# Kernel optimization log

Measured on AMD Instinct MI355X. Metric: run time of the kernel, lower is better.

## Reference

```python
import jax, jax.numpy as jnp
import numpy as np

N, F_IN, H, C, E, G, OUT = 50000, 128, 4, 64, 800000, 128, 8

def _glorot(key, shape):
    lim = float(np.sqrt(6.0 / (shape[0] + shape[-1] if len(shape) == 2 else shape[-1] + 1)))
    return jax.random.uniform(key, shape, jnp.float32, -lim, lim)

def setup_inputs() -> dict:
    key = jax.random.key(0)
    ks = jax.random.split(key, 12)
    x = jax.random.normal(ks[0], (N, F_IN), jnp.float32)
    edge_index = jax.random.randint(ks[1], (2, E), 0, N, jnp.int64)
    batch = jnp.sort(jax.random.randint(ks[2], (N,), 0, G, jnp.int64))
    return {
        "x": x, "edge_index": edge_index, "batch": batch,
        "W1": _glorot(ks[3], (F_IN, H * C)),
        "a1s": _glorot(ks[4], (H, C)), "a1d": _glorot(ks[5], (H, C)),
        "b1": jnp.zeros((H * C,), jnp.float32),
        "W2": _glorot(ks[6], (H * C, H * C)),
        "a2s": _glorot(ks[7], (H, C)), "a2d": _glorot(ks[8], (H, C)),
        "b2": jnp.zeros((C,), jnp.float32),
        "fc_w": _glorot(ks[9], (C, OUT)),
        "fc_b": jnp.zeros((OUT,), jnp.float32),
    }

def _gat_conv(x, src, dst, W, a_src, a_dst, bias, concat):
    # x: [N, in]; src/dst: [E'] (self-loops already appended, PyG default)
    n = x.shape[0]
    h = (x @ W).reshape(n, H, C)                       # [N, H, C]
    alpha_src = (h * a_src).sum(-1)                    # [N, H]
    alpha_dst = (h * a_dst).sum(-1)                    # [N, H]
    e = alpha_src[src] + alpha_dst[dst]                # [E', H]
    e = jax.nn.leaky_relu(e, 0.2)
    # neighbor softmax grouped by destination node
    m = jax.ops.segment_max(e, dst, num_segments=n)    # [N, H]
    ex = jnp.exp(e - m[dst])
    denom = jax.ops.segment_sum(ex, dst, num_segments=n)
    alpha = ex / (denom[dst] + 1e-16)                  # [E', H]
    msg = h[src] * alpha[:, :, None]                   # [E', H, C]
    out = jax.ops.segment_sum(msg, dst, num_segments=n)  # [N, H, C]
    out = out.reshape(n, H * C) if concat else out.mean(axis=1)
    return out + bias

def reference(x, edge_index, batch, W1, a1s, a1d, b1, W2, a2s, a2d, b2, fc_w, fc_b):
    n = x.shape[0]
    loop = jnp.arange(n, dtype=edge_index.dtype)
    src = jnp.concatenate([edge_index[0], loop])
    dst = jnp.concatenate([edge_index[1], loop])
    h = _gat_conv(x, src, dst, W1, a1s, a1d, b1, concat=True)
    h = jax.nn.elu(h)                                  # activation, dropout p=0
    h = _gat_conv(h, src, dst, W2, a2s, a2d, b2, concat=False)
    # global mean pool over graphs
    sums = jax.ops.segment_sum(h, batch, num_segments=G)
    cnts = jax.ops.segment_sum(jnp.ones((n,), h.dtype), batch, num_segments=G)
    pooled = sums / jnp.maximum(cnts, 1.0)[:, None]    # [G, C]
    return pooled @ fc_w + fc_b                        # [G, OUT]
```

## Files before the change

kernel.cpp:

```cpp
#include <hip/hip_runtime.h>
#include <hip/hip_bf16.h>
#include <cstddef>
#include <cstdint>

#define NN 50000
#define MPAD 50048
#define F_IN 128
#define NH 4
#define NC 64
#define NE 800000
#define NG 128
#define NOUT 8
#define HC 256
#define EP (NE + NN)

typedef unsigned short ushort_t;
typedef _Float16 f16;
typedef __attribute__((ext_vector_type(2))) _Float16 f16x2;
typedef __attribute__((ext_vector_type(8))) _Float16 f16x8;
typedef __attribute__((ext_vector_type(4))) float f32x4;

__device__ __forceinline__ float lrelu02(float x) { return x > 0.0f ? x : 0.2f * x; }
__device__ __forceinline__ float elu1(float x)    { return x > 0.0f ? x : expm1f(x); }

__device__ __forceinline__ ushort_t f2h_bits(float f) {
    f16 h = (f16)f;
    union { f16 h; ushort_t u; } cv; cv.h = h;
    return cv.u;
}
__device__ __forceinline__ uint32_t pack2h(float a, float b) {
    union { f16 h[2]; uint32_t u; } cv;
    cv.h[0] = (f16)a; cv.h[1] = (f16)b;
    return cv.u;
}
__device__ __forceinline__ f16x2 as_h2(uint32_t q) {
    union { uint32_t u; f16x2 h; } cv; cv.u = q;
    return cv.h;
}
__device__ __forceinline__ void h2_unpack(uint32_t q, float& lo, float& hi) {
    union { uint32_t u; f16 h[2]; } cv; cv.u = q;
    lo = (float)cv.h[0];
    hi = (float)cv.h[1];
}

__device__ __forceinline__ float fdot2f(f16x2 a, f16x2 b, float c) {
#if __has_builtin(__builtin_amdgcn_fdot2)
    return __builtin_amdgcn_fdot2(a, b, c, false);
#else
    float d;
    asm("v_dot2_f32_f16 %0, %1, %2, %3" : "=v"(d) : "v"(a), "v"(b), "v"(c));
    return d;
#endif
}
__device__ __forceinline__ uint32_t permb(uint32_t a, uint32_t b, uint32_t s) {
    return __builtin_amdgcn_perm(a, b, s);
}
#define SEL_E 0x01000504u
#define SEL_O 0x03020706u

__device__ __forceinline__ void gld16(const void* g, void* l) {
    __builtin_amdgcn_global_load_lds(
        (const __attribute__((address_space(1))) unsigned int*)g,
        (__attribute__((address_space(3))) unsigned int*)l, 16, 0, 0);
}

#define XN4 (NN * F_IN / 4)
#define NW (F_IN * HC + HC * HC)
__global__ void prep_kernel(const int* __restrict__ edst,
                            const float* __restrict__ x,
                            const float* __restrict__ W1,
                            const float* __restrict__ W2,
                            int* __restrict__ deg,
                            f16* __restrict__ xh,
                            f16* __restrict__ w1t, f16* __restrict__ w2t) {
    int idx = blockIdx.x * blockDim.x + threadIdx.x;
    if (idx < EP) {
        int d = (idx < NE) ? edst[idx] : (idx - NE);
        atomicAdd(&deg[d], 1);
        return;
    }
    idx -= EP;
    if (idx < XN4) {
        float4 v = ((const float4*)x)[idx];
        f16 o[4] = {(f16)v.x, (f16)v.y, (f16)v.z, (f16)v.w};
        *(uint2*)(xh + idx * 4) = *(const uint2*)o;
        return;
    }
    idx -= XN4;
    const int n1 = F_IN * HC;
    if (idx < n1) {
        int k = idx / HC, n = idx % HC;
        w1t[n * F_IN + k] = (f16)W1[idx];
    } else if (idx < NW) {
        int i2 = idx - n1;
        int k = i2 / HC, n = i2 % HC;
        w2t[n * HC + k] = (f16)W2[i2];
    }
}

__global__ __launch_bounds__(256) void scan_p1(const int* __restrict__ deg,
                                               int* __restrict__ partials) {
    __shared__ int lds[256];
    int b = blockIdx.x, t = threadIdx.x;
    int i0 = b * 1024 + t * 4;
    int s = 0;
#pragma unroll
    for (int j = 0; j < 4; j++) { int i = i0 + j; if (i < NN) s += deg[i]; }
    lds[t] = s;
    __syncthreads();
    for (int o = 128; o; o >>= 1) { if (t < o) lds[t] += lds[t + o]; __syncthreads(); }
    if (t == 0) partials[b] = lds[0];
}

__global__ __launch_bounds__(256) void scan_p3(const int* __restrict__ deg,
                                               const int* __restrict__ partials,
                                               int* __restrict__ offs) {
    __shared__ int lds[256];
    __shared__ int base_s;
    int b = blockIdx.x, t = threadIdx.x;
    if (t == 0) {
        int s = 0;
        for (int i = 0; i < b; i++) s += partials[i];
        base_s = s;
        if (b == 0) offs[0] = 0;
    }
    int i0 = b * 1024 + t * 4;
    int v[4]; int s = 0;
#pragma unroll
    for (int j = 0; j < 4; j++) { int i = i0 + j; v[j] = (i < NN) ? deg[i] : 0; s += v[j]; }
    lds[t] = s;
    __syncthreads();
    for (int o = 1; o < 256; o <<= 1) {
        int x = (t >= o) ? lds[t - o] : 0;
        __syncthreads();
        lds[t] += x;
        __syncthreads();
    }
    int run = base_s + (lds[t] - s);
#pragma unroll
    for (int j = 0; j < 4; j++) { run += v[j]; int i = i0 + j; if (i < NN) offs[i + 1] = run; }
}

__global__ void edge_fill(const int* __restrict__ esrc, const int* __restrict__ edst,
                          const int* __restrict__ offs, int* __restrict__ fill,
                          int* __restrict__ csr) {
    int e = blockIdx.x * blockDim.x + threadIdx.x;
    if (e >= EP) return;
    int s, d;
    if (e < NE) { s = esrc[e]; d = edst[e]; } else { s = d = e - NE; }
    int pos = offs[d] + atomicAdd(&fill[d], 1);
    csr[pos] = s;
}

__global__ __launch_bounds__(256, 3) void gemm_gat(
        const f16* __restrict__ A, const f16* __restrict__ BT,
        const float* __restrict__ a_s, const float* __restrict__ a_d,
        ushort_t* __restrict__ hf2, float* __restrict__ asrc,
        float* __restrict__ adst, int M, int K) {
    __shared__ alignas(16) char smem[33792];
    f16* lA = (f16*)smem;
    f16* lB = (f16*)smem + 4096;

    int t = threadIdx.x;
    int wave = t >> 6, lane = t & 63;
    int wm = wave >> 1, wn = wave & 1;
    int quad = lane >> 4, l15 = lane & 15;
    int tileM = blockIdx.x * 128;
    int by = blockIdx.y;

    f32x4 acc[4][4];
#pragma unroll
    for (int f = 0; f < 4; f++)
#pragma unroll
        for (int g = 0; g < 4; g++) acc[f][g] = (f32x4){0.f, 0.f, 0.f, 0.f};

    for (int k0 = 0; k0 < K; k0 += 32) {
        __syncthreads();
#pragma unroll
        for (int i = 0; i < 2; i++) {
            int c = wave * 2 + i;
            int row = c * 16 + (lane >> 2);
            int kk = k0 + (lane & 3) * 8;
            gld16(A + (size_t)(tileM + row) * K + kk, &lA[c * 512]);
            gld16(BT + (size_t)(by * 128 + row) * K + kk, &lB[c * 512]);
        }
        __syncthreads();

        f16x8 ah[4], bh[4];
#pragma unroll
        for (int f = 0; f < 4; f++)
            ah[f] = *(const f16x8*)&lA[(wm * 64 + f * 16 + l15) * 32 + quad * 8];
#pragma unroll
        for (int g = 0; g < 4; g++)
            bh[g] = *(const f16x8*)&lB[(wn * 64 + g * 16 + l15) * 32 + quad * 8];
#pragma unroll
        for (int f = 0; f < 4; f++)
#pragma unroll
            for (int g = 0; g < 4; g++)
                acc[f][g] = __builtin_amdgcn_mfma_f32_16x16x32_f16(ah[f], bh[g], acc[f][g], 0, 0, 0);
    }

    int head = (by << 1) | wn;
    float as_v[4], ad_v[4];
#pragma unroll
    for (int g = 0; g < 4; g++) {
        as_v[g] = a_s[head * 64 + g * 16 + l15];
        ad_v[g] = a_d[head * 64 + g * 16 + l15];
    }
#pragma unroll
    for (int f = 0; f < 4; f++) {
#pragma unroll
        for (int r = 0; r < 4; r++) {
            float ps = acc[f][0][r] * as_v[0] + acc[f][1][r] * as_v[1]
                     + acc[f][2][r] * as_v[2] + acc[f][3][r] * as_v[3];
            float pd = acc[f][0][r] * ad_v[0] + acc[f][1][r] * ad_v[1]
                     + acc[f][2][r] * ad_v[2] + acc[f][3][r] * ad_v[3];
#pragma unroll
            for (int o = 1; o < 16; o <<= 1) {
                ps += __shfl_xor(ps, o);
                pd += __shfl_xor(pd, o);
            }
            int row = tileM + wm * 64 + f * 16 + quad * 4 + r;
            if (l15 == 0 && row < M) {
                asrc[row * 4 + head] = ps;
                adst[row * 4 + head] = pd;
            }
        }
    }

    __syncthreads();
    ushort_t* lC2u = (ushort_t*)smem;
    const uint32_t* lC2d = (const uint32_t*)smem;
#pragma unroll
    for (int f = 0; f < 4; f++)
#pragma unroll
        for (int g = 0; g < 4; g++)
#pragma unroll
            for (int r = 0; r < 4; r++)
                lC2u[(wm * 64 + f * 16 + quad * 4 + r) * 132 + (g * 16 + l15) * 2 + wn] =
                    f2h_bits(acc[f][g][r]);
    __syncthreads();
    uint32_t* hb2 = (uint32_t*)hf2;
#pragma unroll
    for (int it = 0; it < 32; it++) {
        int row = wave * 32 + it;
        uint32_t v = lC2d[row * 66 + lane];
        hb2[(size_t)(tileM + row) * 128 + by * 64 + lane] = v;
    }
}

template <int CONCAT>
__global__ __launch_bounds__(256) void gat_agg(const ushort_t* __restrict__ hf2,
                                               const float* __restrict__ asrc,
                                               const float* __restrict__ adst,
                                               const int* __restrict__ offs,
                                               const int* __restrict__ csr,
                                               const float* __restrict__ bias,
                                               f16* __restrict__ oh,
                                               float* __restrict__ of) {
    __shared__ uint2 lw[4][64];
    int wave = threadIdx.x >> 6, lane = threadIdx.x & 63;
    int node = blockIdx.x * 4 + wave;
    if (node >= NN) return;
    int start = offs[node];
    int deg = offs[node + 1] - start;
    float4 ad = *(const float4*)(adst + node * 4);

    float w0, w1, w2, w3;
    float m0, m1, m2, m3, i0, i1, i2, i3;
    int msrc = 0;

    if (deg <= 64) {
        float t0 = -1e30f, t1 = -1e30f, t2 = -1e30f, t3 = -1e30f;
        if (lane < deg) {
            int sidx = csr[start + lane];
            float4 as = *(const float4*)(asrc + sidx * 4);
            t0 = lrelu02(as.x + ad.x);
            t1 = lrelu02(as.y + ad.y);
            t2 = lrelu02(as.z + ad.z);
            t3 = lrelu02(as.w + ad.w);
            msrc = sidx;
        }
        m0 = t0; m1 = t1; m2 = t2; m3 = t3;
#pragma unroll
        for (int o = 1; o < 64; o <<= 1) {
            m0 = fmaxf(m0, __shfl_xor(m0, o));
            m1 = fmaxf(m1, __shfl_xor(m1, o));
            m2 = fmaxf(m2, __shfl_xor(m2, o));
            m3 = fmaxf(m3, __shfl_xor(m3, o));
        }
        w0 = __expf(t0 - m0);
        w1 = __expf(t1 - m1);
        w2 = __expf(t2 - m2);
        w3 = __expf(t3 - m3);
        float s0 = w0, s1 = w1, s2 = w2, s3 = w3;
#pragma unroll
        for (int o = 1; o < 64; o <<= 1) {
            s0 += __shfl_xor(s0, o);
            s1 += __shfl_xor(s1, o);
            s2 += __shfl_xor(s2, o);
            s3 += __shfl_xor(s3, o);
        }
        i0 = 1.0f / (s0 + 1e-16f);
        i1 = 1.0f / (s1 + 1e-16f);
        i2 = 1.0f / (s2 + 1e-16f);
        i3 = 1.0f / (s3 + 1e-16f);
        w0 *= i0; w1 *= i1; w2 *= i2; w3 *= i3;
    } else {
        m0 = m1 = m2 = m3 = -1e30f;
        float s0 = 0.f, s1 = 0.f, s2 = 0.f, s3 = 0.f;
        float e0 = 0.f, e1 = 0.f, e2 = 0.f, e3 = 0.f;
        for (int j = lane; j < deg; j += 64) {
            int sidx = csr[start + j];
            float4 as = *(const float4*)(asrc + sidx * 4);
            float t0 = lrelu02(as.x + ad.x);
            float t1 = lrelu02(as.y + ad.y);
            float t2 = lrelu02(as.z + ad.z);
            float t3 = lrelu02(as.w + ad.w);
            if (j == lane) { e0 = t0; e1 = t1; e2 = t2; e3 = t3; msrc = sidx; }
            float nm;
            nm = fmaxf(m0, t0); s0 = s0 * __expf(m0 - nm) + __expf(t0 - nm); m0 = nm;
            nm = fmaxf(m1, t1); s1 = s1 * __expf(m1 - nm) + __expf(t1 - nm); m1 = nm;
            nm = fmaxf(m2, t2); s2 = s2 * __expf(m2 - nm) + __expf(t2 - nm); m2 = nm;
            nm = fmaxf(m3, t3); s3 = s3 * __expf(m3 - nm) + __expf(t3 - nm); m3 = nm;
        }
        for (int o = 32; o; o >>= 1) {
            float om, os, nm;
            om = __shfl_xor(m0, o); os = __shfl_xor(s0, o);
            nm = fmaxf(m0, om); s0 = s0 * __expf(m0 - nm) + os * __expf(om - nm); m0 = nm;
            om = __shfl_xor(m1, o); os = __shfl_xor(s1, o);
            nm = fmaxf(m1, om); s1 = s1 * __expf(m1 - nm) + os * __expf(om - nm); m1 = nm;
            om = __shfl_xor(m2, o); os = __shfl_xor(s2, o);
            nm = fmaxf(m2, om); s2 = s2 * __expf(m2 - nm) + os * __expf(om - nm); m2 = nm;
            om = __shfl_xor(m3, o); os = __shfl_xor(s3, o);
            nm = fmaxf(m3, om); s3 = s3 * __expf(m3 - nm) + os * __expf(om - nm); m3 = nm;
        }
        i0 = 1.0f / (s0 + 1e-16f);
        i1 = 1.0f / (s1 + 1e-16f);
        i2 = 1.0f / (s2 + 1e-16f);
        i3 = 1.0f / (s3 + 1e-16f);
        w0 = __expf(e0 - m0) * i0;
        w1 = __expf(e1 - m1) * i1;
        w2 = __expf(e2 - m2) * i2;
        w3 = __expf(e3 - m3) * i3;
    }

    lw[wave][lane] = (uint2){pack2h(w0, w1), pack2h(w2, w3)};

    int hp = lane >> 5;
    const uint32_t* lwu = (const uint32_t*)&lw[wave][0];
    float aE0 = 0.f, aO0 = 0.f, aE1 = 0.f, aO1 = 0.f;
    float c0a = 0.f, c0b = 0.f, c1a = 0.f, c1b = 0.f;
    const uint32_t* hb = (const uint32_t*)hf2 + lane * 2;
    int jmax = deg < 64 ? deg : 64;

    int j = 0;
    if (CONCAT) {
        for (; j + 4 <= jmax; j += 4) {
            int s0 = __builtin_amdgcn_readlane(msrc, j);
            int s1 = __builtin_amdgcn_readlane(msrc, j + 1);
            int s2 = __builtin_amdgcn_readlane(msrc, j + 2);
            int s3 = __builtin_amdgcn_readlane(msrc, j + 3);
            uint2 q0 = *(const uint2*)(hb + (size_t)s0 * 128);
            uint2 q1 = *(const uint2*)(hb + (size_t)s1 * 128);
            uint2 q2 = *(const uint2*)(hb + (size_t)s2 * 128);
            uint2 q3 = *(const uint2*)(hb + (size_t)s3 * 128);
            uint32_t wA = lwu[(j + 0) * 2 + hp];
            uint32_t wB = lwu[(j + 1) * 2 + hp];
            uint32_t wC = lwu[(j + 2) * 2 + hp];
            uint32_t wD = lwu[(j + 3) * 2 + hp];
            uint32_t weAB = permb(wA, wB, SEL_E), woAB = permb(wA, wB, SEL_O);
            uint32_t weCD = permb(wC, wD, SEL_E), woCD = permb(wC, wD, SEL_O);
            uint32_t xeAB = permb(q0.x, q1.x, SEL_E), xoAB = permb(q0.x, q1.x, SEL_O);
            uint32_t yeAB = permb(q0.y, q1.y, SEL_E), yoAB = permb(q0.y, q1.y, SEL_O);
            uint32_t xeCD = permb(q2.x, q3.x, SEL_E), xoCD = permb(q2.x, q3.x, SEL_O);
            uint32_t yeCD = permb(q2.y, q3.y, SEL_E), yoCD = permb(q2.y, q3.y, SEL_O);
            aE0 = fdot2f(as_h2(xeAB), as_h2(weAB), aE0);
            aO0 = fdot2f(as_h2(xoAB), as_h2(woAB), aO0);
            aE1 = fdot2f(as_h2(yeAB), as_h2(weAB), aE1);
            aO1 = fdot2f(as_h2(yoAB), as_h2(woAB), aO1);
            aE0 = fdot2f(as_h2(xeCD), as_h2(weCD), aE0);
            aO0 = fdot2f(as_h2(xoCD), as_h2(woCD), aO0);
            aE1 = fdot2f(as_h2(yeCD), as_h2(weCD), aE1);
            aO1 = fdot2f(as_h2(yoCD), as_h2(woCD), aO1);
        }
        for (; j < jmax; j++) {
            int sidx = __builtin_amdgcn_readlane(msrc, j);
            f16x2 wh = as_h2(lwu[j * 2 + hp]);
            uint2 q = *(const uint2*)(hb + (size_t)sidx * 128);
            f16x2 qx = as_h2(q.x), qy = as_h2(q.y);
            aE0 += (float)qx[0] * (float)wh[0];
            aO0 += (float)qx[1] * (float)wh[1];
            aE1 += (float)qy[0] * (float)wh[0];
            aO1 += (float)qy[1] * (float)wh[1];
        }
    } else {
        for (; j + 4 <= jmax; j += 4) {
            int s0 = __builtin_amdgcn_readlane(msrc, j);
            int s1 = __builtin_amdgcn_readlane(msrc, j + 1);
            int s2 = __builtin_amdgcn_readlane(msrc, j + 2);
            int s3 = __builtin_amdgcn_readlane(msrc, j + 3);
            uint2 q0 = *(const uint2*)(hb + (size_t)s0 * 128);
            uint2 q1 = *(const uint2*)(hb + (size_t)s1 * 128);
            uint2 q2 = *(const uint2*)(hb + (size_t)s2 * 128);
            uint2 q3 = *(const uint2*)(hb + (size_t)s3 * 128);
            f16x2 w0v = as_h2(lwu[(j + 0) * 2 + hp]);
            f16x2 w1v = as_h2(lwu[(j + 1) * 2 + hp]);
            f16x2 w2v = as_h2(lwu[(j + 2) * 2 + hp]);
            f16x2 w3v = as_h2(lwu[(j + 3) * 2 + hp]);
            c0a = fdot2f(as_h2(q0.x), w0v, c0a);
            c1a = fdot2f(as_h2(q0.y), w0v, c1a);
            c0b = fdot2f(as_h2(q1.x), w1v, c0b);
            c1b = fdot2f(as_h2(q1.y), w1v, c1b);
            c0a = fdot2f(as_h2(q2.x), w2v, c0a);
            c1a = fdot2f(as_h2(q2.y), w2v, c1a);
            c0b = fdot2f(as_h2(q3.x), w3v, c0b);
            c1b = fdot2f(as_h2(q3.y), w3v, c1b);
        }
        for (; j < jmax; j++) {
            int sidx = __builtin_amdgcn_readlane(msrc, j);
            f16x2 wh = as_h2(lwu[j * 2 + hp]);
            uint2 q = *(const uint2*)(hb + (size_t)sidx * 128);
            c0a = fdot2f(as_h2(q.x), wh, c0a);
            c1a = fdot2f(as_h2(q.y), wh, c1a);
        }
    }
    for (int jj = 64; jj < deg; jj++) {
        int sidx = csr[start + jj];
        float4 as = *(const float4*)(asrc + sidx * 4);
        float u0 = __expf(lrelu02(as.x + ad.x) - m0) * i0;
        float u1 = __expf(lrelu02(as.y + ad.y) - m1) * i1;
        float u2 = __expf(lrelu02(as.z + ad.z) - m2) * i2;
        float u3 = __expf(lrelu02(as.w + ad.w) - m3) * i3;
        float ue = hp ? u2 : u0;
        float uo = hp ? u3 : u1;
        uint2 q = *(const uint2*)(hb + (size_t)sidx * 128);
        float xl, xh2, yl, yh;
        h2_unpack(q.x, xl, xh2);
        h2_unpack(q.y, yl, yh);
        if (CONCAT) {
            aE0 += ue * xl;
            aO0 += uo * xh2;
            aE1 += ue * yl;
            aO1 += uo * yh;
        } else {
            c0a += ue * xl + uo * xh2;
            c1a += ue * yl + uo * yh;
        }
    }

    int c0 = (lane & 31) * 2;
    int he = hp * 2, ho = hp * 2 + 1;
    if (CONCAT) {
        size_t base = (size_t)node * HC;
        float vE0 = elu1(aE0 + bias[he * 64 + c0]);
        float vE1 = elu1(aE1 + bias[he * 64 + c0 + 1]);
        float vO0 = elu1(aO0 + bias[ho * 64 + c0]);
        float vO1 = elu1(aO1 + bias[ho * 64 + c0 + 1]);
        f16 pe[2] = {(f16)vE0, (f16)vE1};
        f16 po[2] = {(f16)vO0, (f16)vO1};
        *(uint32_t*)(oh + base + he * 64 + c0) = *(const uint32_t*)pe;
        *(uint32_t*)(oh + base + ho * 64 + c0) = *(const uint32_t*)po;
    } else {
        float s0 = c0a + c0b;
        float s1 = c1a + c1b;
        s0 += __shfl_xor(s0, 32);
        s1 += __shfl_xor(s1, 32);
        if (hp == 0) {
            float2 v = {0.25f * s0 + bias[c0], 0.25f * s1 + bias[c0 + 1]};
            *(float2*)(of + (size_t)node * NC + c0) = v;
        }
    }
}

__global__ __launch_bounds__(256) void pool_kernel(const float* __restrict__ out2,
                                                   const int* __restrict__ batch,
                                                   float* __restrict__ pool,
                                                   float* __restrict__ cnt) {
    int gw = (blockIdx.x * blockDim.x + threadIdx.x) >> 6;
    int lane = threadIdx.x & 63;
    int start = gw * 16;
    if (start >= NN) return;
    int end = start + 16 < NN ? start + 16 : NN;
    int curg = batch[start];
    float acc = 0.f; int run = 0;
    for (int node = start; node < end; node++) {
        int g = batch[node];
        if (g != curg) {
            atomicAdd(&pool[curg * 64 + lane], acc);
            if (lane == 0) atomicAdd(&cnt[curg], (float)run);
            curg = g; acc = 0.f; run = 0;
        }
        acc += out2[(size_t)node * NC + lane];
        run++;
    }
    atomicAdd(&pool[curg * 64 + lane], acc);
    if (lane == 0) atomicAdd(&cnt[curg], (float)run);
}

__global__ void fc_kernel(const float* __restrict__ pool, const float* __restrict__ cnt,
                          const float* __restrict__ fc_w, const float* __restrict__ fc_b,
                          float* __restrict__ out) {
    int idx = blockIdx.x * blockDim.x + threadIdx.x;
    if (idx >= NG * NOUT) return;
    int g = idx >> 3, o = idx & 7;
    float inv = 1.0f / fmaxf(cnt[g], 1.0f);
    float s = 0.f;
#pragma unroll
    for (int c = 0; c < 64; c++) s += pool[g * 64 + c] * fc_w[c * 8 + o];
    out[idx] = s * inv + fc_b[o];
}

extern "C" void kernel_launch(void* const* d_in, const int* in_sizes, int n_in,
                              void* d_out, int out_size, void* d_ws, size_t ws_size,
                              hipStream_t stream) {
    const float* x    = (const float*)d_in[0];
    const int*   ei   = (const int*)d_in[1];
    const int*   batch= (const int*)d_in[2];
    const float* W1   = (const float*)d_in[3];
    const float* a1s  = (const float*)d_in[4];
    const float* a1d  = (const float*)d_in[5];
    const float* b1   = (const float*)d_in[6];
    const float* W2   = (const float*)d_in[7];
    const float* a2s  = (const float*)d_in[8];
    const float* a2d  = (const float*)d_in[9];
    const float* b2   = (const float*)d_in[10];
    const float* fc_w = (const float*)d_in[11];
    const float* fc_b = (const float*)d_in[12];
    float* out = (float*)d_out;

    char* p = (char*)d_ws;
    auto alloc = [&](size_t bytes) -> char* {
        char* r = p; p += (bytes + 255) & ~(size_t)255; return r;
    };
    int*   deg     = (int*)alloc((size_t)NN * 4);
    int*   fill    = (int*)alloc((size_t)NN * 4);
    float* pool    = (float*)alloc((size_t)NG * 64 * 4);
    float* cnt     = (float*)alloc((size_t)NG * 4);
    size_t zero_bytes = (size_t)(p - (char*)d_ws);
    int*   offs    = (int*)alloc((size_t)(NN + 1) * 4);
    int*   partials= (int*)alloc(64 * 4);
    int*   csr     = (int*)alloc((size_t)EP * 4);
    float* asrc    = (float*)alloc((size_t)NN * 4 * 4);
    float* adst    = (float*)alloc((size_t)NN * 4 * 4);
    ushort_t* hf2  = (ushort_t*)alloc((size_t)MPAD * HC * 2);
    f16*   xh      = (f16*)alloc((size_t)MPAD * F_IN * 2);
    f16*   act     = (f16*)alloc((size_t)MPAD * HC * 2);
    f16*   w1t     = (f16*)alloc((size_t)HC * F_IN * 2);
    f16*   w2t     = (f16*)alloc((size_t)HC * HC * 2);
    float* out2    = (float*)xh;

    hipMemsetAsync(d_ws, 0, zero_bytes, stream);

    int prep_n = EP + XN4 + NW;
    prep_kernel<<<(prep_n + 255) / 256, 256, 0, stream>>>(
        ei + NE, x, W1, W2, deg, xh, w1t, w2t);
    scan_p1<<<49, 256, 0, stream>>>(deg, partials);
    scan_p3<<<49, 256, 0, stream>>>(deg, partials, offs);
    edge_fill<<<(EP + 255) / 256, 256, 0, stream>>>(ei, ei + NE, offs, fill, csr);

    dim3 gg((NN + 127) / 128, HC / 128);
    int nb4 = (NN + 3) / 4;

    gemm_gat<<<gg, 256, 0, stream>>>(xh, w1t, a1s, a1d, hf2, asrc, adst, NN, F_IN);
    gat_agg<1><<<nb4, 256, 0, stream>>>(hf2, asrc, adst, offs, csr, b1, act, nullptr);
    gemm_gat<<<gg, 256, 0, stream>>>(act, w2t, a2s, a2d, hf2, asrc, adst, NN, HC);
    gat_agg<0><<<nb4, 256, 0, stream>>>(hf2, asrc, adst, offs, csr, b2, nullptr, out2);
    pool_kernel<<<((NN + 15) / 16 + 3) / 4, 256, 0, stream>>>(out2, batch, pool, cnt);
    fc_kernel<<<(NG * NOUT + 255) / 256, 256, 0, stream>>>(pool, cnt, fc_w, fc_b, out);
}
```

Before: 376.1 us.

## Process two nodes per wavefront in GAT aggregation with half-wave 16-byte gathers

The aggregation kernel now assigns two destination nodes per 64-lane wave. Each 32-lane half handles one node's softmax and gathers 16-byte feature chunks per lane. If either node in a wave has degree above 32, the wave falls back to the old full-wave per-node routine for both nodes. Average degree is about 17, so most waves take the half-wave path, which should reduce idle lanes and per-node overhead. The cost is branch divergence on the fallback path, and rows near NN may be read without a bounds check (offs and the padded buffers may cover it).

```diff
diff --git a/kernel.cpp b/kernel.cpp
--- a/kernel.cpp
+++ b/kernel.cpp
@@ -250,18 +250,15 @@
 }
 
 template <int CONCAT>
-__global__ __launch_bounds__(256) void gat_agg(const ushort_t* __restrict__ hf2,
-                                               const float* __restrict__ asrc,
-                                               const float* __restrict__ adst,
-                                               const int* __restrict__ offs,
-                                               const int* __restrict__ csr,
-                                               const float* __restrict__ bias,
-                                               f16* __restrict__ oh,
-                                               float* __restrict__ of) {
-    __shared__ uint2 lw[4][64];
-    int wave = threadIdx.x >> 6, lane = threadIdx.x & 63;
-    int node = blockIdx.x * 4 + wave;
-    if (node >= NN) return;
+__device__ void gat_node_fullwave(const ushort_t* __restrict__ hf2,
+                                  const float* __restrict__ asrc,
+                                  const float* __restrict__ adst,
+                                  const int* __restrict__ offs,
+                                  const int* __restrict__ csr,
+                                  const float* __restrict__ bias,
+                                  f16* __restrict__ oh,
+                                  float* __restrict__ of,
+                                  int node, int lane, uint2* lwF) {
     int start = offs[node];
     int deg = offs[node + 1] - start;
     float4 ad = *(const float4*)(adst + node * 4);
@@ -345,10 +342,10 @@
         w3 = __expf(e3 - m3) * i3;
     }
 
-    lw[wave][lane] = (uint2){pack2h(w0, w1), pack2h(w2, w3)};
+    lwF[lane] = (uint2){pack2h(w0, w1), pack2h(w2, w3)};
 
     int hp = lane >> 5;
-    const uint32_t* lwu = (const uint32_t*)&lw[wave][0];
+    const uint32_t* lwu = (const uint32_t*)lwF;
     float aE0 = 0.f, aO0 = 0.f, aE1 = 0.f, aO1 = 0.f;
     float c0a = 0.f, c0b = 0.f, c1a = 0.f, c1b = 0.f;
     const uint32_t* hb = (const uint32_t*)hf2 + lane * 2;
@@ -473,6 +470,159 @@
     }
 }
 
+template <int CONCAT>
+__global__ __launch_bounds__(256) void gat_agg(const ushort_t* __restrict__ hf2,
+                                               const float* __restrict__ asrc,
+                                               const float* __restrict__ adst,
+                                               const int* __restrict__ offs,
+                                               const int* __restrict__ csr,
+                                               const float* __restrict__ bias,
+                                               f16* __restrict__ oh,
+                                               float* __restrict__ of) {
+    __shared__ uint4 lw4[4][64];
+    int wave = threadIdx.x >> 6, lane = threadIdx.x & 63;
+    int grp = lane >> 5, l31 = lane & 31;
+    int hp = (lane >> 4) & 1;
+    int nbase = blockIdx.x * 8 + wave * 2;
+    int node = nbase + grp;
+    int start = offs[node];
+    int deg = offs[node + 1] - start;
+
+    if (!__all(deg <= 32)) {
+        uint2* lwF = (uint2*)&lw4[wave][0];
+        gat_node_fullwave<CONCAT>(hf2, asrc, adst, offs, csr, bias, oh, of,
+                                  nbase, lane, lwF);
+        gat_node_fullwave<CONCAT>(hf2, asrc, adst, offs, csr, bias, oh, of,
+                                  nbase + 1, lane, lwF);
+        return;
+    }
+
+    float4 ad = *(const float4*)(adst + (size_t)node * 4);
+    float t0 = -1e30f, t1 = -1e30f, t2 = -1e30f, t3 = -1e30f;
+    int msrc = 0;
+    if (l31 < deg) {
+        int sidx = csr[start + l31];
+        float4 as = *(const float4*)(asrc + (size_t)sidx * 4);
+        t0 = lrelu02(as.x + ad.x);
+        t1 = lrelu02(as.y + ad.y);
+        t2 = lrelu02(as.z + ad.z);
+        t3 = lrelu02(as.w + ad.w);
+        msrc = sidx;
+    }
+    float m0 = t0, m1 = t1, m2 = t2, m3 = t3;
+#pragma unroll
+    for (int o = 1; o < 32; o <<= 1) {
+        m0 = fmaxf(m0, __shfl_xor(m0, o));
+        m1 = fmaxf(m1, __shfl_xor(m1, o));
+        m2 = fmaxf(m2, __shfl_xor(m2, o));
+        m3 = fmaxf(m3, __shfl_xor(m3, o));
+    }
+    float w0 = __expf(t0 - m0);
+    float w1 = __expf(t1 - m1);
+    float w2 = __expf(t2 - m2);
+    float w3 = __expf(t3 - m3);
+    float s0 = w0, s1 = w1, s2 = w2, s3 = w3;
+#pragma unroll
+    for (int o = 1; o < 32; o <<= 1) {
+        s0 += __shfl_xor(s0, o);
+        s1 += __shfl_xor(s1, o);
+        s2 += __shfl_xor(s2, o);
+        s3 += __shfl_xor(s3, o);
+    }
+    w0 *= 1.0f / (s0 + 1e-16f);
+    w1 *= 1.0f / (s1 + 1e-16f);
+    w2 *= 1.0f / (s2 + 1e-16f);
+    w3 *= 1.0f / (s3 + 1e-16f);
+
+    lw4[wave][lane] = (uint4){(uint32_t)msrc, pack2h(w0, w1),
+                              (uint32_t)msrc, pack2h(w2, w3)};
+
+    const uint2* lwp = (const uint2*)&lw4[wave][grp * 32];
+    const uint4* hq = (const uint4*)hf2;
+    int c0 = (l31 & 15) * 4;
+
+    if (CONCAT) {
+        float aE0 = 0.f, aE1 = 0.f, aE2 = 0.f, aE3 = 0.f;
+        float aO0 = 0.f, aO1 = 0.f, aO2 = 0.f, aO3 = 0.f;
+        int j = 0;
+        for (; j + 2 <= deg; j += 2) {
+            uint2 e0 = lwp[(j + 0) * 2 + hp];
+            uint2 e1 = lwp[(j + 1) * 2 + hp];
+            uint4 q0 = hq[(size_t)e0.x * 32 + l31];
+            uint4 q1 = hq[(size_t)e1.x * 32 + l31];
+            uint32_t we = permb(e0.y, e1.y, SEL_E);
+            uint32_t wo = permb(e0.y, e1.y, SEL_O);
+            aE0 = fdot2f(as_h2(permb(q0.x, q1.x, SEL_E)), as_h2(we), aE0);
+            aO0 = fdot2f(as_h2(permb(q0.x, q1.x, SEL_O)), as_h2(wo), aO0);
+            aE1 = fdot2f(as_h2(permb(q0.y, q1.y, SEL_E)), as_h2(we), aE1);
+            aO1 = fdot2f(as_h2(permb(q0.y, q1.y, SEL_O)), as_h2(wo), aO1);
+            aE2 = fdot2f(as_h2(permb(q0.z, q1.z, SEL_E)), as_h2(we), aE2);
+            aO2 = fdot2f(as_h2(permb(q0.z, q1.z, SEL_O)), as_h2(wo), aO2);
+            aE3 = fdot2f(as_h2(permb(q0.w, q1.w, SEL_E)), as_h2(we), aE3);
+            aO3 = fdot2f(as_h2(permb(q0.w, q1.w, SEL_O)), as_h2(wo), aO3);
+        }
+        if (j < deg) {
+            uint2 e0 = lwp[j * 2 + hp];
+            uint4 q0 = hq[(size_t)e0.x * 32 + l31];
+            f16x2 wh = as_h2(e0.y);
+            f16x2 v;
+            v = as_h2(q0.x); aE0 += (float)v[0] * (float)wh[0]; aO0 += (float)v[1] * (float)wh[1];
+            v = as_h2(q0.y); aE1 += (float)v[0] * (float)wh[0]; aO1 += (float)v[1] * (float)wh[1];
+            v = as_h2(q0.z); aE2 += (float)v[0] * (float)wh[0]; aO2 += (float)v[1] * (float)wh[1];
+            v = as_h2(q0.w); aE3 += (float)v[0] * (float)wh[0]; aO3 += (float)v[1] * (float)wh[1];
+        }
+        int he = hp * 2, ho = hp * 2 + 1;
+        size_t base = (size_t)node * HC;
+        float4 bE = *(const float4*)(bias + he * 64 + c0);
+        float4 bO = *(const float4*)(bias + ho * 64 + c0);
+        f16 pe[4] = {(f16)elu1(aE0 + bE.x), (f16)elu1(aE1 + bE.y),
+                     (f16)elu1(aE2 + bE.z), (f16)elu1(aE3 + bE.w)};
+        f16 po[4] = {(f16)elu1(aO0 + bO.x), (f16)elu1(aO1 + bO.y),
+                     (f16)elu1(aO2 + bO.z), (f16)elu1(aO3 + bO.w)};
+        *(uint2*)(oh + base + he * 64 + c0) = *(const uint2*)pe;
+        *(uint2*)(oh + base + ho * 64 + c0) = *(const uint2*)po;
+    } else {
+        float a0 = 0.f, a1 = 0.f, a2 = 0.f, a3 = 0.f;
+        float b0 = 0.f, b1 = 0.f, b2 = 0.f, b3 = 0.f;
+        int j = 0;
+        for (; j + 2 <= deg; j += 2) {
+            uint2 e0 = lwp[(j + 0) * 2 + hp];
+            uint2 e1 = lwp[(j + 1) * 2 + hp];
+            uint4 q0 = hq[(size_t)e0.x * 32 + l31];
+            uint4 q1 = hq[(size_t)e1.x * 32 + l31];
+            f16x2 wv0 = as_h2(e0.y), wv1 = as_h2(e1.y);
+            a0 = fdot2f(as_h2(q0.x), wv0, a0);
+            a1 = fdot2f(as_h2(q0.y), wv0, a1);
+            a2 = fdot2f(as_h2(q0.z), wv0, a2);
+            a3 = fdot2f(as_h2(q0.w), wv0, a3);
+            b0 = fdot2f(as_h2(q1.x), wv1, b0);
+            b1 = fdot2f(as_h2(q1.y), wv1, b1);
+            b2 = fdot2f(as_h2(q1.z), wv1, b2);
+            b3 = fdot2f(as_h2(q1.w), wv1, b3);
+        }
+        if (j < deg) {
+            uint2 e0 = lwp[j * 2 + hp];
+            uint4 q0 = hq[(size_t)e0.x * 32 + l31];
+            f16x2 wv0 = as_h2(e0.y);
+            a0 = fdot2f(as_h2(q0.x), wv0, a0);
+            a1 = fdot2f(as_h2(q0.y), wv0, a1);
+            a2 = fdot2f(as_h2(q0.z), wv0, a2);
+            a3 = fdot2f(as_h2(q0.w), wv0, a3);
+        }
+        float u0 = a0 + b0, u1 = a1 + b1, u2 = a2 + b2, u3 = a3 + b3;
+        u0 += __shfl_xor(u0, 16);
+        u1 += __shfl_xor(u1, 16);
+        u2 += __shfl_xor(u2, 16);
+        u3 += __shfl_xor(u3, 16);
+        if (hp == 0) {
+            float4 bv = *(const float4*)(bias + c0);
+            float4 v = {0.25f * u0 + bv.x, 0.25f * u1 + bv.y,
+                        0.25f * u2 + bv.z, 0.25f * u3 + bv.w};
+            *(float4*)(of + (size_t)node * NC + c0) = v;
+        }
+    }
+}
+
 __global__ __launch_bounds__(256) void pool_kernel(const float* __restrict__ out2,
                                                    const int* __restrict__ batch,
                                                    float* __restrict__ pool,
@@ -560,12 +710,12 @@
     edge_fill<<<(EP + 255) / 256, 256, 0, stream>>>(ei, ei + NE, offs, fill, csr);
 
     dim3 gg((NN + 127) / 128, HC / 128);
-    int nb4 = (NN + 3) / 4;
+    int nb8 = (NN + 7) / 8;
 
     gemm_gat<<<gg, 256, 0, stream>>>(xh, w1t, a1s, a1d, hf2, asrc, adst, NN, F_IN);
-    gat_agg<1><<<nb4, 256, 0, stream>>>(hf2, asrc, adst, offs, csr, b1, act, nullptr);
+    gat_agg<1><<<nb8, 256, 0, stream>>>(hf2, asrc, adst, offs, csr, b1, act, nullptr);
     gemm_gat<<<gg, 256, 0, stream>>>(act, w2t, a2s, a2d, hf2, asrc, adst, NN, HC);
-    gat_agg<0><<<nb4, 256, 0, stream>>>(hf2, asrc, adst, offs, csr, b2, nullptr, out2);
+    gat_agg<0><<<nb8, 256, 0, stream>>>(hf2, asrc, adst, offs, csr, b2, nullptr, out2);
     pool_kernel<<<((NN + 15) / 16 + 3) / 4, 256, 0, stream>>>(out2, batch, pool, cnt);
     fc_kernel<<<(NG * NOUT + 255) / 256, 256, 0, stream>>>(pool, cnt, fc_w, fc_b, out);
 }
```

Measured after the change: 370.6 us. No clear change (-1.5%).
